# Kernel optimization log

Hardware: AMD Instinct MI355X
Metric: run time of the kernel (lower is better)

The kernel has to match this reference:

```python
import jax, jax.numpy as jnp
import numpy as np
from jax.scipy.special import logsumexp

BUCKET_SIZE = 64
N_HASHES = 8
TOKEN_SELF_ATTN_VALUE = -50000.0


def setup_inputs() -> dict:
    key = jax.random.key(0)
    k1, k2, k3 = jax.random.split(key, 3)
    B, T, H, E = 2, 4096, 8, 64
    n_buckets = T // BUCKET_SIZE  # 64
    qk = jax.random.normal(k1, (B, T, H, E), dtype=jnp.float32)
    v = jax.random.normal(k2, (B, T, H, E), dtype=jnp.float32)
    # random rotations for LSH hashing: (E, n_hashes, n_buckets//2)
    rotations = jax.random.normal(k3, (E, N_HASHES, n_buckets // 2), dtype=jnp.float32)
    return {"qk": qk, "v": v, "rotations": rotations}


def reference(qk, v, rotations):
    B, T, H, E = qk.shape
    D = v.shape[-1]
    bs = BUCKET_SIZE
    nh = N_HASHES
    n_buckets = T // bs
    BH = B * H
    softmax_temp = 1.0 / jnp.sqrt(jnp.float32(E))

    # (b t h e) -> (b h) t e
    qkf = qk.transpose(0, 2, 1, 3).reshape(BH, T, E)
    vf = v.transpose(0, 2, 1, 3).reshape(BH, T, D)

    # --- hash_vectors ---
    # rotated: (BH, nh, T, n_buckets//2)
    rotated = jnp.einsum('btf,fhi->bhti', qkf, rotations)
    rotated = jnp.concatenate([rotated, -rotated], axis=-1)  # (BH, nh, T, n_buckets)
    buckets = jnp.argmax(rotated, axis=-1)  # (BH, nh, T)
    buckets = buckets.transpose(1, 0, 2)    # (nh, BH, T)

    # stable sort into buckets
    perm = jnp.argsort(buckets, axis=-1)       # stable by default; (nh, BH, T)
    perm_inv = jnp.argsort(perm, axis=-1)      # inverse permutation

    # look-one-back on kv indices
    p = perm.reshape(nh, BH, n_buckets, bs)
    p_prev = jnp.roll(p, 1, axis=2)            # cat([x[:,-1:], x[:,:-1]]) == roll by 1
    perm_ob = jnp.concatenate([p, p_prev], axis=3)  # (nh, BH, n_buckets, 2*bs)

    def gather_seq(x, idx_flat):
        # x: (BH, T, d), idx_flat: (nh, BH, S') -> (nh, BH, S', d)
        return jnp.take_along_axis(x[None], idx_flat[..., None], axis=2)

    qk_norm = qkf / jnp.linalg.norm(qkf, axis=-1, keepdims=True)

    tq = gather_seq(qkf, perm).reshape(nh, BH, n_buckets, bs, E)
    tk = gather_seq(qk_norm, perm_ob.reshape(nh, BH, -1)).reshape(nh, BH, n_buckets, 2 * bs, E)
    tv = gather_seq(vf, perm_ob.reshape(nh, BH, -1)).reshape(nh, BH, n_buckets, 2 * bs, D)

    inner = jnp.einsum('hbnie,hbnje->hbnij', tq, tk) * softmax_temp

    bq_idx = p[..., :, None]                       # (nh, BH, n_buckets, bs, 1)
    bkv_idx = perm_ob[..., None, :]                # (nh, BH, n_buckets, 1, 2*bs)
    inner = jnp.where(bq_idx == bkv_idx, TOKEN_SELF_ATTN_VALUE, inner)

    lse = logsumexp(inner, axis=-1, keepdims=True)  # (nh, BH, n_buckets, bs, 1)
    dots = jnp.exp(inner - lse)
    so = jnp.einsum('hbnij,hbnjd->hbnid', dots, tv)  # (nh, BH, n_buckets, bs, D)

    # unsort back to original token order
    o = jnp.take_along_axis(so.reshape(nh, BH, T, D), perm_inv[..., None], axis=2)
    logits = jnp.take_along_axis(lse.reshape(nh, BH, T, 1), perm_inv[..., None], axis=2)

    # combine the n_hashes rounds with softmax weights over the hash axis
    probs = jax.nn.softmax(logits, axis=0)
    out = jnp.sum(o * probs, axis=0)  # (BH, T, D)
    out = out.reshape(B, H, T, D).transpose(0, 2, 1, 3)  # (B, T, H, D)
    return out
```

## Files before the change

### kernel.cpp

```cpp
#include <hip/hip_runtime.h>
#include <hip/hip_bf16.h>
#include <hip/hip_fp16.h>
#include <math.h>

#define T 4096
#define NH 8
#define BHN 16
#define NB 64
#define BS 64

using f16x8 = __attribute__((ext_vector_type(8))) _Float16;
using fp16x2_builtin = __attribute__((ext_vector_type(2))) __fp16;
using f32x4 = __attribute__((ext_vector_type(4))) float;

__device__ __forceinline__ f32x4 mfma16f(f16x8 a, f16x8 b, f32x4 c) {
  return __builtin_amdgcn_mfma_f32_16x16x32_f16(a, b, c, 0, 0, 0);
}

__device__ __forceinline__ float fast_exp2(float x) {
  return __builtin_amdgcn_exp2f(x);
}

__device__ __forceinline__ unsigned cvtpk_f16(float a, float b) {
  fp16x2_builtin r = __builtin_amdgcn_cvt_pkrtz(a, b);
  unsigned u; __builtin_memcpy(&u, &r, 4); return u;
}
__device__ __forceinline__ unsigned pk_h2_rn(float a, float b) {
  __half2 h = __float22half2_rn(make_float2(a, b));
  unsigned u; __builtin_memcpy(&u, &h, 4); return u;
}
__device__ __forceinline__ float f4get(const float4& v, int i) {
  return i == 0 ? v.x : i == 1 ? v.y : i == 2 ? v.z : v.w;
}
__device__ __forceinline__ unsigned u4get(const uint4& v, int i) {
  return i == 0 ? v.x : i == 1 ? v.y : i == 2 ? v.z : v.w;
}

__device__ __forceinline__ void async_load16(const void* src, void* dst_lds) {
  __builtin_amdgcn_global_load_lds(
      (const __attribute__((address_space(1))) unsigned int*)src,
      (__attribute__((address_space(3))) unsigned int*)dst_lds, 16, 0, 0);
}

#define SWZ128(row, inb) ((((row)) << 7) + ((inb) ^ ((((row)) & 7) << 4)))
#define SWZ256(row, inb) ((((row)) << 8) + ((inb) ^ ((((row)) & 7) << 4)))

__global__ __launch_bounds__(256) void k_prepbkt(const float* __restrict__ qk,
                                                 const float* __restrict__ v,
                                                 const float* __restrict__ rot,
                                                 unsigned short* __restrict__ khf,
                                                 unsigned short* __restrict__ vhf,
                                                 float* __restrict__ norm025,
                                                 unsigned char* __restrict__ buckets) {
  __shared__ float sQ[64][65];
  const int tid = threadIdx.x;
  const int t0 = blockIdx.x * 64;
  const int bh = blockIdx.y;
  const int b = bh >> 3, hh = bh & 7;
  const size_t gbase = (size_t)b * ((size_t)T * 512) + (size_t)hh * 64;

  #pragma unroll
  for (int i = 0; i < 4; ++i) {
    int rr = i * 16 + (tid >> 4);
    int cc = (tid & 15) * 4;
    float4 x = *(const float4*)&qk[gbase + (size_t)(t0 + rr) * 512 + cc];
    sQ[rr][cc] = x.x; sQ[rr][cc + 1] = x.y; sQ[rr][cc + 2] = x.z; sQ[rr][cc + 3] = x.w;
  }
  __syncthreads();

  {
    const int tok = tid >> 2, q4 = tid & 3;
    float x[16];
    #pragma unroll
    for (int k = 0; k < 16; ++k) x[k] = sQ[tok][q4 * 16 + k];
    float4 y[4];
    const size_t gv = gbase + (size_t)(t0 + tok) * 512 + q4 * 16;
    #pragma unroll
    for (int k = 0; k < 4; ++k) y[k] = *(const float4*)&v[gv + k * 4];

    float ss = 0.f;
    #pragma unroll
    for (int k = 0; k < 16; ++k) ss += x[k] * x[k];
    ss += __shfl_xor(ss, 1);
    ss += __shfl_xor(ss, 2);
    const float invn = rsqrtf(ss);

    const size_t ob = ((size_t)bh * T + (t0 + tok)) * 64 + q4 * 16;
    unsigned kw[8], vw[8];
    #pragma unroll
    for (int p = 0; p < 8; ++p) {
      kw[p] = pk_h2_rn(x[2 * p] * invn, x[2 * p + 1] * invn);
      vw[p] = pk_h2_rn(f4get(y[p >> 1], (p & 1) * 2), f4get(y[p >> 1], (p & 1) * 2 + 1));
    }
    *(uint4*)&khf[ob]     = (uint4){kw[0], kw[1], kw[2], kw[3]};
    *(uint4*)&khf[ob + 8] = (uint4){kw[4], kw[5], kw[6], kw[7]};
    *(uint4*)&vhf[ob]     = (uint4){vw[0], vw[1], vw[2], vw[3]};
    *(uint4*)&vhf[ob + 8] = (uint4){vw[4], vw[5], vw[6], vw[7]};
    if (q4 == 0) norm025[(size_t)bh * T + (t0 + tok)] = 0.125f * ss * invn;
  }

  const int wv = __builtin_amdgcn_readfirstlane(tid >> 6);
  const int tok = tid & 63;
  const int t = t0 + tok;

  float a0[32], a1[32];
  #pragma unroll
  for (int i = 0; i < 32; ++i) { a0[i] = 0.f; a1[i] = 0.f; }
  for (int f = 0; f < 64; ++f) {
    float qv = sQ[tok][f];
    const float* rp = rot + (size_t)f * (NH * 32) + wv * 64;
    #pragma unroll
    for (int i = 0; i < 32; ++i) {
      a0[i] = fmaf(qv, rp[i], a0[i]);
      a1[i] = fmaf(qv, rp[32 + i], a1[i]);
    }
  }
  #pragma unroll
  for (int h = 0; h < 2; ++h) {
    const float* ac = h ? a1 : a0;
    float maxv = -INFINITY, minv = INFINITY;
    int amax = 0, amin = 0;
    #pragma unroll
    for (int i = 0; i < 32; ++i) {
      if (ac[i] > maxv) { maxv = ac[i]; amax = i; }
      if (ac[i] < minv) { minv = ac[i]; amin = i; }
    }
    int bucket = (maxv >= -minv) ? amax : 32 + amin;
    buckets[((size_t)(2 * wv + h) * BHN + bh) * T + t] = (unsigned char)bucket;
  }
}

__global__ __launch_bounds__(1024) void k_sort(const unsigned char* __restrict__ buckets,
                                               int* __restrict__ perm) {
  __shared__ unsigned short bkt[T];
  __shared__ unsigned short rnk[T];
  __shared__ unsigned int cnt[64 * 64];
  __shared__ unsigned int bbase[64];
  __shared__ unsigned int btot[64];

  const int tid = threadIdx.x;
  const int seg = blockIdx.x;
  const unsigned char* bin = buckets + (size_t)seg * T;

  for (int idx = tid; idx < T; idx += 1024) bkt[idx] = bin[idx];
  #pragma unroll
  for (int i = 0; i < 4; ++i) cnt[tid + i * 1024] = 0;
  __syncthreads();

  const int wave = tid >> 6, lane = tid & 63;
  const unsigned long long lt = (1ull << lane) - 1ull;
  #pragma unroll
  for (int cc = 0; cc < 4; ++cc) {
    int chunk = wave * 4 + cc;
    int e = bkt[chunk * 64 + lane];
    unsigned long long m = ~0ull;
    #pragma unroll
    for (int bb = 0; bb < 6; ++bb) {
      unsigned long long mb = __ballot(((e >> bb) & 1) != 0);
      m &= ((e >> bb) & 1) ? mb : ~mb;
    }
    unsigned long long below = m & lt;
    rnk[chunk * 64 + lane] = (unsigned short)__popcll(below);
    if (below == 0ull)
      cnt[e * 64 + chunk] = (unsigned int)__popcll(m);
  }
  __syncthreads();
  if (tid < 64) {
    unsigned int run = 0;
    for (int c = 0; c < 64; ++c) {
      unsigned int v = cnt[tid * 64 + c];
      cnt[tid * 64 + c] = run;
      run += v;
    }
    btot[tid] = run;
  }
  __syncthreads();
  if (tid == 0) {
    unsigned int run = 0;
    for (int bb = 0; bb < 64; ++bb) { bbase[bb] = run; run += btot[bb]; }
  }
  __syncthreads();
  for (int idx = tid; idx < T; idx += 1024) {
    int e = bkt[idx];
    int c = idx >> 6;
    int pos = (int)(bbase[e] + cnt[e * 64 + c] + rnk[idx]);
    perm[(size_t)seg * T + pos] = idx;
  }
}

__global__ __launch_bounds__(256, 5) void k_attn15(
    const unsigned short* __restrict__ khf, const unsigned short* __restrict__ vhf,
    const int* __restrict__ perm, const float* __restrict__ norm025,
    __half* __restrict__ o_ws, float* __restrict__ lsum_ws) {
  __shared__ __align__(16) char smem[32768];
  constexpr int LK  = 0;
  constexpr int LP  = 0;
  constexpr int LVT = 16384;

  const int tid = threadIdx.x;
  const int wg = ((int)blockIdx.x & 7) * 1024 + ((int)blockIdx.x >> 3);
  const int n = wg & 63, bh = (wg >> 6) & 15, r = wg >> 10;
  const size_t rowbase = (size_t)bh * T;
  const size_t ps = ((size_t)r * BHN + bh) * T;
  const int base_own = n * 64;
  const int base_prev = ((n + 63) & 63) * 64;

  const int wid = tid >> 6, lane = tid & 63;
  const int lr = lane & 15, lg = lane >> 4;

  const int qtok = perm[ps + base_own + 16 * wid + lr];
  const float scale = norm025[rowbase + qtok];

  const int vj0 = (tid & 63) * 2;
  const int vd0 = (tid >> 6) * 16;
  int vt[2];
  #pragma unroll
  for (int j = 0; j < 2; ++j) {
    int src = (vj0 + j < 64) ? (base_own + vj0 + j) : (base_prev + vj0 + j - 64);
    vt[j] = perm[ps + src];
  }
  uint4 VA0, VA1, VB0, VB1;
  {
    const uint4* pa = (const uint4*)&vhf[(rowbase + (size_t)vt[0]) * 64 + vd0];
    const uint4* pb = (const uint4*)&vhf[(rowbase + (size_t)vt[1]) * 64 + vd0];
    VA0 = pa[0]; VA1 = pa[1];
    VB0 = pb[0]; VB1 = pb[1];
  }

  #pragma unroll
  for (int it = 0; it < 4; ++it) {
    int unit = it * 256 + tid;
    int row = unit >> 3, sl = unit & 7;
    int ssl = sl ^ (row & 7);
    int src = (row < 64) ? (base_own + row) : (base_prev + (row - 64));
    int tokr = perm[ps + src];
    async_load16(&khf[(rowbase + (size_t)tokr) * 64 + ssl * 8], smem + LK + unit * 16);
  }
  __syncthreads();

  f16x8 bq[2];
  #pragma unroll
  for (int ks = 0; ks < 2; ++ks)
    bq[ks] = *(const f16x8*)(smem + LK + SWZ128(16 * wid + lr, lg * 16 + ks * 64));

  f32x4 c[8];
  #pragma unroll
  for (int t = 0; t < 8; ++t) c[t] = (f32x4){0.f, 0.f, 0.f, 0.f};
  #pragma unroll
  for (int t = 0; t < 8; ++t) {
    #pragma unroll
    for (int ks = 0; ks < 2; ++ks) {
      f16x8 ak = *(const f16x8*)(smem + LK + SWZ128(16 * t + lr, lg * 16 + ks * 64));
      c[t] = mfma16f(ak, bq[ks], c[t]);
    }
  }

  #pragma unroll
  for (int dd = 0; dd < 16; ++dd) {
    unsigned aw = (dd < 8) ? u4get(VA0, dd >> 1) : u4get(VA1, (dd - 8) >> 1);
    unsigned bw = (dd < 8) ? u4get(VB0, dd >> 1) : u4get(VB1, (dd - 8) >> 1);
    unsigned w = (dd & 1) ? __builtin_amdgcn_perm(bw, aw, 0x07060302u)
                          : __builtin_amdgcn_perm(bw, aw, 0x05040100u);
    *(unsigned*)(smem + LVT + SWZ256(vd0 + dd, vj0 * 2)) = w;
  }

  #pragma unroll
  for (int t = 0; t < 4; ++t) {
    #pragma unroll
    for (int rr = 0; rr < 4; ++rr)
      if (16 * t + 4 * lg + rr == 16 * wid + lr) c[t][rr] = -1e30f;
  }

  const float sl2e = scale * 1.4426950408889634f;
  float ll = 0.f;
  #pragma unroll
  for (int t = 0; t < 8; ++t) {
    #pragma unroll
    for (int rr = 0; rr < 4; ++rr) {
      float e = fast_exp2(c[t][rr] * sl2e);
      c[t][rr] = e;
      ll += e;
    }
  }
  ll += __shfl_xor(ll, 16);
  ll += __shfl_xor(ll, 32);
  if (lg == 0) lsum_ws[ps + qtok] = ll;

  __syncthreads();

  {
    const int prow = 16 * wid + lr;
    #pragma unroll
    for (int t = 0; t < 8; ++t) {
      unsigned u01 = cvtpk_f16(c[t][0], c[t][1]);
      unsigned u23 = cvtpk_f16(c[t][2], c[t][3]);
      *(uint2*)(smem + LP + SWZ256(prow, 32 * t + 8 * lg)) = make_uint2(u01, u23);
    }
  }
  __syncthreads();

  f16x8 pa[4];
  #pragma unroll
  for (int ks = 0; ks < 4; ++ks)
    pa[ks] = *(const f16x8*)(smem + LP + SWZ256(16 * wid + lr, ks * 64 + lg * 16));
  f32x4 o[4];
  #pragma unroll
  for (int td = 0; td < 4; ++td) o[td] = (f32x4){0.f, 0.f, 0.f, 0.f};
  #pragma unroll
  for (int td = 0; td < 4; ++td) {
    #pragma unroll
    for (int ks = 0; ks < 4; ++ks) {
      f16x8 bv = *(const f16x8*)(smem + LVT + SWZ256(16 * td + lr, lg * 16 + ks * 64));
      o[td] = mfma16f(pa[ks], bv, o[td]);
    }
  }

  #pragma unroll
  for (int rr = 0; rr < 4; ++rr) {
    int otok = __shfl(qtok, 4 * lg + rr);
    size_t gb = (ps + (size_t)otok) * 64 + lr;
    #pragma unroll
    for (int td = 0; td < 4; ++td)
      o_ws[gb + 16 * td] = __float2half(o[td][rr]);
  }
}

__global__ __launch_bounds__(256) void k_combine(const __half* __restrict__ o_ws,
                                                 const float* __restrict__ lsum_ws,
                                                 float* __restrict__ out) {
  const int gid = blockIdx.x * 256 + threadIdx.x;
  const int d4 = (gid & 15) * 4;
  const int row = gid >> 4;
  const int bh = row >> 12;
  const int t = row & (T - 1);

  float lsum = 0.f;
  #pragma unroll
  for (int r = 0; r < 8; ++r)
    lsum += lsum_ws[((size_t)r * BHN + bh) * T + t];
  float rcp = 1.0f / lsum;

  float a0 = 0.f, a1 = 0.f, a2 = 0.f, a3 = 0.f;
  #pragma unroll
  for (int r = 0; r < 8; ++r) {
    const __half* op = &o_ws[(((size_t)r * BHN + bh) * T + t) * 64 + d4];
    __half2 h01 = *(const __half2*)&op[0];
    __half2 h23 = *(const __half2*)&op[2];
    float2 f01 = __half22float2(h01);
    float2 f23 = __half22float2(h23);
    a0 += f01.x; a1 += f01.y;
    a2 += f23.x; a3 += f23.y;
  }
  const int b = bh >> 3, hh = bh & 7;
  *(float4*)&out[(((size_t)b * T + t) * 8 + hh) * 64 + d4] =
      make_float4(a0 * rcp, a1 * rcp, a2 * rcp, a3 * rcp);
}

extern "C" void kernel_launch(void* const* d_in, const int* in_sizes, int n_in,
                              void* d_out, int out_size, void* d_ws, size_t ws_size,
                              hipStream_t stream) {
  const float* qk  = (const float*)d_in[0];
  const float* v   = (const float*)d_in[1];
  const float* rot = (const float*)d_in[2];
  float* out = (float*)d_out;

  char* ws = (char*)d_ws;
  __half* o_ws          = (__half*)(ws);
  int* perm             = (int*)(ws + 67108864);
  unsigned char* bkts   = (unsigned char*)(ws + 75497472);
  float* lsum_ws        = (float*)(ws + 76021760);
  float* norm025        = (float*)(ws + 78118912);
  unsigned short* khf   = (unsigned short*)(ws + 78381056);
  unsigned short* vhf   = (unsigned short*)(ws + 86769664);

  k_prepbkt<<<dim3(T / 64, BHN), 256, 0, stream>>>(qk, v, rot, khf, vhf, norm025, bkts);
  k_sort<<<dim3(NH * BHN), 1024, 0, stream>>>(bkts, perm);
  k_attn15<<<dim3(NB * BHN * NH), 256, 0, stream>>>(khf, vhf, perm, norm025,
                                                    o_ws, lsum_ws);
  k_combine<<<dim3((BHN * T * 16) / 256), 256, 0, stream>>>(o_ws, lsum_ws, out);
}
```

Baseline: 111.1 us.

## Process two buckets per attention block with prefetch overlap and wider combine loads

Each attention workgroup now handles two adjacent buckets instead of one. The K/V gathers for the second bucket are issued while the first bucket's PV matmul runs, and the P tile reuses the K buffer region. MFMA sections get raised wave priority via s_setprio. The combine kernel reads 8 halves per thread with 16-byte loads. The aim is to halve the block count and hide gather latency, at the cost of fewer blocks for occupancy, more registers and extra barriers.

```diff
diff --git a/kernel.cpp b/kernel.cpp
--- a/kernel.cpp
+++ b/kernel.cpp
@@ -188,43 +188,48 @@
   }
 }
 
-__global__ __launch_bounds__(256, 5) void k_attn15(
+__global__ __launch_bounds__(256, 5) void k_attn16(
     const unsigned short* __restrict__ khf, const unsigned short* __restrict__ vhf,
     const int* __restrict__ perm, const float* __restrict__ norm025,
     __half* __restrict__ o_ws, float* __restrict__ lsum_ws) {
   __shared__ __align__(16) char smem[32768];
   constexpr int LK  = 0;
-  constexpr int LP  = 0;
   constexpr int LVT = 16384;
 
   const int tid = threadIdx.x;
-  const int wg = ((int)blockIdx.x & 7) * 1024 + ((int)blockIdx.x >> 3);
-  const int n = wg & 63, bh = (wg >> 6) & 15, r = wg >> 10;
+  const int wg = ((int)blockIdx.x & 7) * 512 + ((int)blockIdx.x >> 3);
+  const int m = wg & 31, bh = (wg >> 5) & 15, r = wg >> 9;
   const size_t rowbase = (size_t)bh * T;
   const size_t ps = ((size_t)r * BHN + bh) * T;
-  const int base_own = n * 64;
-  const int base_prev = ((n + 63) & 63) * 64;
+  const int n0 = 2 * m, n1 = 2 * m + 1;
+  const int b0_own = n0 * 64, b0_prev = ((n0 + 63) & 63) * 64;
+  const int b1_own = n1 * 64, b1_prev = n0 * 64;
 
   const int wid = tid >> 6, lane = tid & 63;
   const int lr = lane & 15, lg = lane >> 4;
-
-  const int qtok = perm[ps + base_own + 16 * wid + lr];
-  const float scale = norm025[rowbase + qtok];
-
   const int vj0 = (tid & 63) * 2;
   const int vd0 = (tid >> 6) * 16;
-  int vt[2];
+
+  const int qtok0 = perm[ps + b0_own + 16 * wid + lr];
+  const float scale0 = norm025[rowbase + qtok0];
+  const int qtok1 = perm[ps + b1_own + 16 * wid + lr];
+  const float scale1 = norm025[rowbase + qtok1];
+
+  int vt0[2], vt1[2];
   #pragma unroll
   for (int j = 0; j < 2; ++j) {
-    int src = (vj0 + j < 64) ? (base_own + vj0 + j) : (base_prev + vj0 + j - 64);
-    vt[j] = perm[ps + src];
-  }
+    int s0 = (vj0 + j < 64) ? (b0_own + vj0 + j) : (b0_prev + vj0 + j - 64);
+    int s1 = (vj0 + j < 64) ? (b1_own + vj0 + j) : (b1_prev + vj0 + j - 64);
+    vt0[j] = perm[ps + s0];
+    vt1[j] = perm[ps + s1];
+  }
+
   uint4 VA0, VA1, VB0, VB1;
   {
-    const uint4* pa = (const uint4*)&vhf[(rowbase + (size_t)vt[0]) * 64 + vd0];
-    const uint4* pb = (const uint4*)&vhf[(rowbase + (size_t)vt[1]) * 64 + vd0];
-    VA0 = pa[0]; VA1 = pa[1];
-    VB0 = pb[0]; VB1 = pb[1];
+    const uint4* pa_ = (const uint4*)&vhf[(rowbase + (size_t)vt0[0]) * 64 + vd0];
+    const uint4* pb_ = (const uint4*)&vhf[(rowbase + (size_t)vt0[1]) * 64 + vd0];
+    VA0 = pa_[0]; VA1 = pa_[1];
+    VB0 = pb_[0]; VB1 = pb_[1];
   }
 
   #pragma unroll
@@ -232,80 +237,104 @@
     int unit = it * 256 + tid;
     int row = unit >> 3, sl = unit & 7;
     int ssl = sl ^ (row & 7);
-    int src = (row < 64) ? (base_own + row) : (base_prev + (row - 64));
+    int src = (row < 64) ? (b0_own + row) : (b0_prev + (row - 64));
     int tokr = perm[ps + src];
     async_load16(&khf[(rowbase + (size_t)tokr) * 64 + ssl * 8], smem + LK + unit * 16);
   }
   __syncthreads();
 
-  f16x8 bq[2];
-  #pragma unroll
-  for (int ks = 0; ks < 2; ++ks)
-    bq[ks] = *(const f16x8*)(smem + LK + SWZ128(16 * wid + lr, lg * 16 + ks * 64));
-
-  f32x4 c[8];
-  #pragma unroll
-  for (int t = 0; t < 8; ++t) c[t] = (f32x4){0.f, 0.f, 0.f, 0.f};
-  #pragma unroll
-  for (int t = 0; t < 8; ++t) {
-    #pragma unroll
-    for (int ks = 0; ks < 2; ++ks) {
-      f16x8 ak = *(const f16x8*)(smem + LK + SWZ128(16 * t + lr, lg * 16 + ks * 64));
-      c[t] = mfma16f(ak, bq[ks], c[t]);
-    }
-  }
-
-  #pragma unroll
-  for (int dd = 0; dd < 16; ++dd) {
-    unsigned aw = (dd < 8) ? u4get(VA0, dd >> 1) : u4get(VA1, (dd - 8) >> 1);
-    unsigned bw = (dd < 8) ? u4get(VB0, dd >> 1) : u4get(VB1, (dd - 8) >> 1);
-    unsigned w = (dd & 1) ? __builtin_amdgcn_perm(bw, aw, 0x07060302u)
-                          : __builtin_amdgcn_perm(bw, aw, 0x05040100u);
-    *(unsigned*)(smem + LVT + SWZ256(vd0 + dd, vj0 * 2)) = w;
-  }
-
-  #pragma unroll
-  for (int t = 0; t < 4; ++t) {
-    #pragma unroll
-    for (int rr = 0; rr < 4; ++rr)
-      if (16 * t + 4 * lg + rr == 16 * wid + lr) c[t][rr] = -1e30f;
-  }
-
-  const float sl2e = scale * 1.4426950408889634f;
-  float ll = 0.f;
-  #pragma unroll
-  for (int t = 0; t < 8; ++t) {
-    #pragma unroll
-    for (int rr = 0; rr < 4; ++rr) {
-      float e = fast_exp2(c[t][rr] * sl2e);
-      c[t][rr] = e;
-      ll += e;
-    }
-  }
-  ll += __shfl_xor(ll, 16);
-  ll += __shfl_xor(ll, 32);
-  if (lg == 0) lsum_ws[ps + qtok] = ll;
-
-  __syncthreads();
+  f32x4 o[4];
+  float ll;
 
   {
-    const int prow = 16 * wid + lr;
+    f16x8 bq[2];
+    #pragma unroll
+    for (int ks = 0; ks < 2; ++ks)
+      bq[ks] = *(const f16x8*)(smem + LK + SWZ128(16 * wid + lr, lg * 16 + ks * 64));
+
+    f32x4 c[8];
+    #pragma unroll
+    for (int t = 0; t < 8; ++t) c[t] = (f32x4){0.f, 0.f, 0.f, 0.f};
+    __builtin_amdgcn_s_setprio(1);
     #pragma unroll
     for (int t = 0; t < 8; ++t) {
-      unsigned u01 = cvtpk_f16(c[t][0], c[t][1]);
-      unsigned u23 = cvtpk_f16(c[t][2], c[t][3]);
-      *(uint2*)(smem + LP + SWZ256(prow, 32 * t + 8 * lg)) = make_uint2(u01, u23);
-    }
-  }
-  __syncthreads();
+      #pragma unroll
+      for (int ks = 0; ks < 2; ++ks) {
+        f16x8 ak = *(const f16x8*)(smem + LK + SWZ128(16 * t + lr, lg * 16 + ks * 64));
+        c[t] = mfma16f(ak, bq[ks], c[t]);
+      }
+    }
+    __builtin_amdgcn_s_setprio(0);
+
+    #pragma unroll
+    for (int dd = 0; dd < 16; ++dd) {
+      unsigned aw = (dd < 8) ? u4get(VA0, dd >> 1) : u4get(VA1, (dd - 8) >> 1);
+      unsigned bw = (dd < 8) ? u4get(VB0, dd >> 1) : u4get(VB1, (dd - 8) >> 1);
+      unsigned w = (dd & 1) ? __builtin_amdgcn_perm(bw, aw, 0x07060302u)
+                            : __builtin_amdgcn_perm(bw, aw, 0x05040100u);
+      *(unsigned*)(smem + LVT + SWZ256(vd0 + dd, vj0 * 2)) = w;
+    }
+
+    #pragma unroll
+    for (int t = 0; t < 4; ++t)
+      #pragma unroll
+      for (int rr = 0; rr < 4; ++rr)
+        if (16 * t + 4 * lg + rr == 16 * wid + lr) c[t][rr] = -1e30f;
+
+    const float sl2e = scale0 * 1.4426950408889634f;
+    ll = 0.f;
+    #pragma unroll
+    for (int t = 0; t < 8; ++t) {
+      #pragma unroll
+      for (int rr = 0; rr < 4; ++rr) {
+        float e = fast_exp2(c[t][rr] * sl2e);
+        c[t][rr] = e;
+        ll += e;
+      }
+    }
+    ll += __shfl_xor(ll, 16);
+    ll += __shfl_xor(ll, 32);
+    if (lg == 0) lsum_ws[ps + qtok0] = ll;
+
+    __syncthreads();
+
+    {
+      const int prow = 16 * wid + lr;
+      #pragma unroll
+      for (int t = 0; t < 8; ++t) {
+        unsigned u01 = cvtpk_f16(c[t][0], c[t][1]);
+        unsigned u23 = cvtpk_f16(c[t][2], c[t][3]);
+        *(uint2*)(smem + LK + SWZ256(prow, 32 * t + 8 * lg)) = make_uint2(u01, u23);
+      }
+    }
+    __syncthreads();
+  }
 
   f16x8 pa[4];
   #pragma unroll
   for (int ks = 0; ks < 4; ++ks)
-    pa[ks] = *(const f16x8*)(smem + LP + SWZ256(16 * wid + lr, ks * 64 + lg * 16));
-  f32x4 o[4];
+    pa[ks] = *(const f16x8*)(smem + LK + SWZ256(16 * wid + lr, ks * 64 + lg * 16));
+  __syncthreads();
+
+  #pragma unroll
+  for (int it = 0; it < 4; ++it) {
+    int unit = it * 256 + tid;
+    int row = unit >> 3, sl = unit & 7;
+    int ssl = sl ^ (row & 7);
+    int src = (row < 64) ? (b1_own + row) : (b1_prev + (row - 64));
+    int tokr = perm[ps + src];
+    async_load16(&khf[(rowbase + (size_t)tokr) * 64 + ssl * 8], smem + LK + unit * 16);
+  }
+  {
+    const uint4* pa_ = (const uint4*)&vhf[(rowbase + (size_t)vt1[0]) * 64 + vd0];
+    const uint4* pb_ = (const uint4*)&vhf[(rowbase + (size_t)vt1[1]) * 64 + vd0];
+    VA0 = pa_[0]; VA1 = pa_[1];
+    VB0 = pb_[0]; VB1 = pb_[1];
+  }
+
   #pragma unroll
   for (int td = 0; td < 4; ++td) o[td] = (f32x4){0.f, 0.f, 0.f, 0.f};
+  __builtin_amdgcn_s_setprio(1);
   #pragma unroll
   for (int td = 0; td < 4; ++td) {
     #pragma unroll
@@ -314,10 +343,102 @@
       o[td] = mfma16f(pa[ks], bv, o[td]);
     }
   }
+  __builtin_amdgcn_s_setprio(0);
 
   #pragma unroll
   for (int rr = 0; rr < 4; ++rr) {
-    int otok = __shfl(qtok, 4 * lg + rr);
+    int otok = __shfl(qtok0, 4 * lg + rr);
+    size_t gb = (ps + (size_t)otok) * 64 + lr;
+    #pragma unroll
+    for (int td = 0; td < 4; ++td)
+      o_ws[gb + 16 * td] = __float2half(o[td][rr]);
+  }
+
+  __syncthreads();
+
+  {
+    f16x8 bq[2];
+    #pragma unroll
+    for (int ks = 0; ks < 2; ++ks)
+      bq[ks] = *(const f16x8*)(smem + LK + SWZ128(16 * wid + lr, lg * 16 + ks * 64));
+
+    f32x4 c[8];
+    #pragma unroll
+    for (int t = 0; t < 8; ++t) c[t] = (f32x4){0.f, 0.f, 0.f, 0.f};
+    __builtin_amdgcn_s_setprio(1);
+    #pragma unroll
+    for (int t = 0; t < 8; ++t) {
+      #pragma unroll
+      for (int ks = 0; ks < 2; ++ks) {
+        f16x8 ak = *(const f16x8*)(smem + LK + SWZ128(16 * t + lr, lg * 16 + ks * 64));
+        c[t] = mfma16f(ak, bq[ks], c[t]);
+      }
+    }
+    __builtin_amdgcn_s_setprio(0);
+
+    #pragma unroll
+    for (int dd = 0; dd < 16; ++dd) {
+      unsigned aw = (dd < 8) ? u4get(VA0, dd >> 1) : u4get(VA1, (dd - 8) >> 1);
+      unsigned bw = (dd < 8) ? u4get(VB0, dd >> 1) : u4get(VB1, (dd - 8) >> 1);
+      unsigned w = (dd & 1) ? __builtin_amdgcn_perm(bw, aw, 0x07060302u)
+                            : __builtin_amdgcn_perm(bw, aw, 0x05040100u);
+      *(unsigned*)(smem + LVT + SWZ256(vd0 + dd, vj0 * 2)) = w;
+    }
+
+    #pragma unroll
+    for (int t = 0; t < 4; ++t)
+      #pragma unroll
+      for (int rr = 0; rr < 4; ++rr)
+        if (16 * t + 4 * lg + rr == 16 * wid + lr) c[t][rr] = -1e30f;
+
+    const float sl2e = scale1 * 1.4426950408889634f;
+    ll = 0.f;
+    #pragma unroll
+    for (int t = 0; t < 8; ++t) {
+      #pragma unroll
+      for (int rr = 0; rr < 4; ++rr) {
+        float e = fast_exp2(c[t][rr] * sl2e);
+        c[t][rr] = e;
+        ll += e;
+      }
+    }
+    ll += __shfl_xor(ll, 16);
+    ll += __shfl_xor(ll, 32);
+    if (lg == 0) lsum_ws[ps + qtok1] = ll;
+
+    __syncthreads();
+
+    {
+      const int prow = 16 * wid + lr;
+      #pragma unroll
+      for (int t = 0; t < 8; ++t) {
+        unsigned u01 = cvtpk_f16(c[t][0], c[t][1]);
+        unsigned u23 = cvtpk_f16(c[t][2], c[t][3]);
+        *(uint2*)(smem + LK + SWZ256(prow, 32 * t + 8 * lg)) = make_uint2(u01, u23);
+      }
+    }
+    __syncthreads();
+  }
+
+  #pragma unroll
+  for (int ks = 0; ks < 4; ++ks)
+    pa[ks] = *(const f16x8*)(smem + LK + SWZ256(16 * wid + lr, ks * 64 + lg * 16));
+  #pragma unroll
+  for (int td = 0; td < 4; ++td) o[td] = (f32x4){0.f, 0.f, 0.f, 0.f};
+  __builtin_amdgcn_s_setprio(1);
+  #pragma unroll
+  for (int td = 0; td < 4; ++td) {
+    #pragma unroll
+    for (int ks = 0; ks < 4; ++ks) {
+      f16x8 bv = *(const f16x8*)(smem + LVT + SWZ256(16 * td + lr, lg * 16 + ks * 64));
+      o[td] = mfma16f(pa[ks], bv, o[td]);
+    }
+  }
+  __builtin_amdgcn_s_setprio(0);
+
+  #pragma unroll
+  for (int rr = 0; rr < 4; ++rr) {
+    int otok = __shfl(qtok1, 4 * lg + rr);
     size_t gb = (ps + (size_t)otok) * 64 + lr;
     #pragma unroll
     for (int td = 0; td < 4; ++td)
@@ -329,8 +450,8 @@
                                                  const float* __restrict__ lsum_ws,
                                                  float* __restrict__ out) {
   const int gid = blockIdx.x * 256 + threadIdx.x;
-  const int d4 = (gid & 15) * 4;
-  const int row = gid >> 4;
+  const int d8 = (gid & 7) * 8;
+  const int row = gid >> 3;
   const int bh = row >> 12;
   const int t = row & (T - 1);
 
@@ -340,20 +461,23 @@
     lsum += lsum_ws[((size_t)r * BHN + bh) * T + t];
   float rcp = 1.0f / lsum;
 
-  float a0 = 0.f, a1 = 0.f, a2 = 0.f, a3 = 0.f;
+  float acc[8];
+  #pragma unroll
+  for (int k = 0; k < 8; ++k) acc[k] = 0.f;
   #pragma unroll
   for (int r = 0; r < 8; ++r) {
-    const __half* op = &o_ws[(((size_t)r * BHN + bh) * T + t) * 64 + d4];
-    __half2 h01 = *(const __half2*)&op[0];
-    __half2 h23 = *(const __half2*)&op[2];
-    float2 f01 = __half22float2(h01);
-    float2 f23 = __half22float2(h23);
-    a0 += f01.x; a1 += f01.y;
-    a2 += f23.x; a3 += f23.y;
+    uint4 u = *(const uint4*)&o_ws[(((size_t)r * BHN + bh) * T + t) * 64 + d8];
+    #pragma unroll
+    for (int k = 0; k < 4; ++k) {
+      __half2 h; __builtin_memcpy(&h, k == 0 ? &u.x : k == 1 ? &u.y : k == 2 ? &u.z : &u.w, 4);
+      float2 f = __half22float2(h);
+      acc[2 * k] += f.x; acc[2 * k + 1] += f.y;
+    }
   }
   const int b = bh >> 3, hh = bh & 7;
-  *(float4*)&out[(((size_t)b * T + t) * 8 + hh) * 64 + d4] =
-      make_float4(a0 * rcp, a1 * rcp, a2 * rcp, a3 * rcp);
+  float* op = &out[(((size_t)b * T + t) * 8 + hh) * 64 + d8];
+  *(float4*)&op[0] = make_float4(acc[0] * rcp, acc[1] * rcp, acc[2] * rcp, acc[3] * rcp);
+  *(float4*)&op[4] = make_float4(acc[4] * rcp, acc[5] * rcp, acc[6] * rcp, acc[7] * rcp);
 }
 
 extern "C" void kernel_launch(void* const* d_in, const int* in_sizes, int n_in,
@@ -375,7 +499,7 @@
 
   k_prepbkt<<<dim3(T / 64, BHN), 256, 0, stream>>>(qk, v, rot, khf, vhf, norm025, bkts);
   k_sort<<<dim3(NH * BHN), 1024, 0, stream>>>(bkts, perm);
-  k_attn15<<<dim3(NB * BHN * NH), 256, 0, stream>>>(khf, vhf, perm, norm025,
-                                                    o_ws, lsum_ws);
-  k_combine<<<dim3((BHN * T * 16) / 256), 256, 0, stream>>>(o_ws, lsum_ws, out);
-}
+  k_attn16<<<dim3((NB / 2) * BHN * NH), 256, 0, stream>>>(khf, vhf, perm, norm025,
+                                                          o_ws, lsum_ws);
+  k_combine<<<dim3((BHN * T * 8) / 256), 256, 0, stream>>>(o_ws, lsum_ws, out);
+}
```

Result: slower. 118.4 us (+6.6%).
